# Optimization experiments

Measured on AMD Instinct MI355X. Metric: run time of the kernel, lower is better.

The kernel has to match this reference:

```python
import jax, jax.numpy as jnp
import numpy as np

BIG_NEG = -1.0e9
B, T, D, C, NF, K = 16, 2048, 64, 32, 16, 20


def setup_inputs() -> dict:
    key = jax.random.key(0)
    ks = jax.random.split(key, 8)
    return {
        "features": jax.random.normal(ks[0], (B, T, D), dtype=jnp.float32),
        "projection_matrix": jax.random.normal(ks[1], (D, NF), dtype=jnp.float32),
        "transition_embs_left": jax.random.normal(ks[2], (C, D), dtype=jnp.float32) * (1.0 / np.sqrt(D)),
        "transition_embs_right": jax.random.normal(ks[3], (C, D), dtype=jnp.float32) * (1.0 / np.sqrt(D)),
        "gaussian_means": jax.random.normal(ks[4], (C, D), dtype=jnp.float32) * 0.1,
        "gaussian_std": jnp.ones((D,), dtype=jnp.float32),
        "poisson_log_rates": jax.random.normal(ks[5], (C,), dtype=jnp.float32) * 0.1,
        "init_logits": jax.random.uniform(ks[6], (C,), dtype=jnp.float32),
        "max_k": K,
    }


def reference(features, projection_matrix, transition_embs_left,
              transition_embs_right, gaussian_means, gaussian_std,
              poisson_log_rates, init_logits, max_k):
    b, t, d = features.shape
    c = gaussian_means.shape[0]

    # --- diagonal-Gaussian per-frame emission log-probs: (B, T, C) ---
    inv_var = 1.0 / (gaussian_std * gaussian_std)              # (D,)
    xx = jnp.einsum("btd,d->bt", features * features, inv_var)  # (B,T)
    xm = jnp.einsum("btd,cd->btc", features, gaussian_means * inv_var)
    mm = jnp.einsum("cd,d->c", gaussian_means * gaussian_means, inv_var)
    quad = xx[:, :, None] - 2.0 * xm + mm[None, None, :]
    log_norm = -jnp.sum(jnp.log(gaussian_std)) - 0.5 * d * jnp.log(2.0 * jnp.pi)
    emission = -0.5 * quad + log_norm                           # (B,T,C)

    # --- sliding-window span sums over lengths 1..max_k (cumsum trick,
    # same math as the unfold+sum in sliding_sum) ---
    cs = jnp.concatenate(
        [jnp.zeros((b, 1, c), dtype=emission.dtype),
         jnp.cumsum(emission, axis=1)], axis=1)                 # (B,T+1,C)
    klens = jnp.arange(1, max_k + 1)                            # (K,)
    ends = jnp.arange(1, t + 1)                                 # (T,)
    starts = ends[None, :] - klens[:, None]                     # (K,T)
    valid = starts >= 0
    span = cs[:, None, ends, :] - jnp.take(cs, jnp.clip(starts, 0), axis=1)
    span = jnp.where(valid[None, :, :, None], span, BIG_NEG)    # (B,K,T,C)

    # --- Poisson length log-pmf per class: (K, C) ---
    kk = klens.astype(emission.dtype)
    length_lp = (kk[:, None] * poisson_log_rates[None, :]
                 - jnp.exp(poisson_log_rates)[None, :]
                 - jax.scipy.special.gammaln(kk + 1.0)[:, None])
    span_scores = span + length_lp[None, :, None, :]            # (B,K,T,C)

    # --- kernelized transition potentials (Performer-style projection;
    # the original kernel creator returns the plain bmm projection) ---
    left = transition_embs_left @ projection_matrix             # (C,NF)
    right = transition_embs_right @ projection_matrix           # (C,NF)
    trans_lp = jax.nn.log_softmax(right @ left.T, axis=0)       # (C_tgt, C_src)

    init_lp = jax.nn.log_softmax(init_logits)                   # (C,)
    return span_scores, trans_lp, init_lp
```

## Files before the change

### kernel.cpp

```cpp
#include <hip/hip_runtime.h>
#include <math.h>

#define BIG_NEG (-1.0e9f)

constexpr int B = 16, T = 2048, D = 64, C = 32, NF = 16;

typedef float f32x4 __attribute__((ext_vector_type(4)));

template<int KT, bool EXACT>
__global__ __launch_bounds__(256) void megakernel(
    const float* __restrict__ feat,
    const float* __restrict__ P,
    const float* __restrict__ TL,
    const float* __restrict__ TR,
    const float* __restrict__ STD,
    const float* __restrict__ MEANS,
    const float* __restrict__ PLR,
    const float* __restrict__ LOGITS,
    float* __restrict__ out,
    float* __restrict__ out_trans,
    float* __restrict__ out_init,
    int Krt)
{
    constexpr int RTOT = 64 + KT;
    constexpr int RPS  = (RTOT + 7) / 8;

    __shared__ float fs[RTOT * 64];
    __shared__ float wm_lds[C * 68];
    __shared__ float iv_lds[64];
    __shared__ float E[RTOT * 33];
    __shared__ float sllp[KT * C];
    __shared__ float slncc[C];
    __shared__ float red[8 * 33];
    __shared__ float lgam[32];
    __shared__ float scc[C];
    __shared__ float sln;

    const int bid = blockIdx.x;
    const int tid = threadIdx.x;
    const int KRUN = EXACT ? KT : Krt;

    if (bid < 512) {
        const int b  = bid & 15;
        const int t0 = (bid >> 4) << 6;

        const float* fb = feat + (size_t)b * T * D;
        constexpr int NF4 = RTOT * 16;
#pragma unroll
        for (int it = 0; it < (NF4 + 255) / 256; ++it) {
            const int idx4 = tid + it * 256;
            if (idx4 < NF4) {
                const int fi  = idx4 * 4;
                const int row = fi >> 6;
                const int col = fi & 63;
                const int t   = t0 - KT + row;
                f32x4 v = {0.f, 0.f, 0.f, 0.f};
                if (t >= 0) v = *(const f32x4*)(fb + (size_t)t * D + col);
                const int cswz = col ^ (((row >> 2) & 7) << 2);
                *(f32x4*)(fs + row * 64 + cswz) = v;
            }
        }
#pragma unroll
        for (int it = 0; it < 2; ++it) {
            const int idx = tid * 4 + it * 1024;
            const int c = idx >> 6, d = idx & 63;
            const f32x4 m = *(const f32x4*)(MEANS + idx);
            const f32x4 s = *(const f32x4*)(STD + d);
            f32x4 w = {m.x / (s.x * s.x), m.y / (s.y * s.y),
                       m.z / (s.z * s.z), m.w / (s.w * s.w)};
            *(f32x4*)(wm_lds + c * 68 + d) = w;
        }
        if (tid < 16) {
            const f32x4 s = *(const f32x4*)(STD + tid * 4);
            f32x4 v = {1.f / (s.x * s.x), 1.f / (s.y * s.y),
                       1.f / (s.z * s.z), 1.f / (s.w * s.w)};
            *(f32x4*)(iv_lds + tid * 4) = v;
        }
        if (tid < 32) {
            float x = (tid >= 1) ? logf((float)(tid + 1)) : 0.f;
#pragma unroll
            for (int off = 1; off < 32; off <<= 1) {
                float vv = __shfl_up(x, off, 64);
                if (tid >= off) x += vv;
            }
            lgam[tid] = x;
        } else if (tid >= 64 && tid < 128) {
            const int l = tid - 64;
            float lg = logf(STD[l]);
#pragma unroll
            for (int off = 1; off < 64; off <<= 1) lg += __shfl_xor(lg, off, 64);
            if (l == 0) sln = -lg - 58.81206612510332f;
        } else if (tid >= 192 && tid < 224) {
            const int c = tid - 192;
            float acc = 0.f;
#pragma unroll
            for (int dq = 0; dq < 64; dq += 4) {
                const f32x4 m = *(const f32x4*)(MEANS + c * 64 + dq);
                const f32x4 s = *(const f32x4*)(STD + dq);
                acc += (m.x * m.x) / (s.x * s.x) + (m.y * m.y) / (s.y * s.y)
                     + (m.z * m.z) / (s.z * s.z) + (m.w * m.w) / (s.w * s.w);
            }
            scc[c] = -0.5f * acc;
        }
        __syncthreads();

        const int j = tid >> 4;
        const float* wr0 = wm_lds + (2 * j) * 68;
        const float* wr1 = wr0 + 68;
#pragma unroll
        for (int pass = 0; pass < 2; ++pass) {
            const int i = (tid & 15) + pass * 16;
            if (pass == 0 || (tid & 15) < (KT / 4)) {
                const int swz = (i & 7) << 2;
                float a0[4] = {0,0,0,0}, a1[4] = {0,0,0,0}, xx[4] = {0,0,0,0};
#pragma unroll
                for (int q = 0; q < 16; ++q) {
                    const int dq = q * 4;
                    const f32x4 w0  = *(const f32x4*)(wr0 + dq);
                    const f32x4 w1  = *(const f32x4*)(wr1 + dq);
                    const f32x4 iv4 = *(const f32x4*)(iv_lds + dq);
                    const int cswz = dq ^ swz;
#pragma unroll
                    for (int tt = 0; tt < 4; ++tt) {
                        const f32x4 f = *(const f32x4*)(fs + (4*i+tt)*64 + cswz);
                        a0[tt] = fmaf(f.x, w0.x, a0[tt]); a0[tt] = fmaf(f.y, w0.y, a0[tt]);
                        a0[tt] = fmaf(f.z, w0.z, a0[tt]); a0[tt] = fmaf(f.w, w0.w, a0[tt]);
                        a1[tt] = fmaf(f.x, w1.x, a1[tt]); a1[tt] = fmaf(f.y, w1.y, a1[tt]);
                        a1[tt] = fmaf(f.z, w1.z, a1[tt]); a1[tt] = fmaf(f.w, w1.w, a1[tt]);
                        xx[tt] = fmaf(f.x * iv4.x, f.x, xx[tt]);
                        xx[tt] = fmaf(f.y * iv4.y, f.y, xx[tt]);
                        xx[tt] = fmaf(f.z * iv4.z, f.z, xx[tt]);
                        xx[tt] = fmaf(f.w * iv4.w, f.w, xx[tt]);
                    }
                }
#pragma unroll
                for (int tt = 0; tt < 4; ++tt) {
                    E[(4*i+tt) * 33 + 2*j]     = a0[tt] - 0.5f * xx[tt];
                    E[(4*i+tt) * 33 + 2*j + 1] = a1[tt] - 0.5f * xx[tt];
                }
            }
        }
        if (tid < C) slncc[tid] = sln + scc[tid];
        for (int e = tid; e < KRUN * C; e += 256) {
            const int k = e >> 5, c = e & 31;
            const float plr = PLR[c];
            sllp[e] = (float)(k + 1) * (plr + sln + scc[c]) - expf(plr) - lgam[k];
        }
        __syncthreads();

        {
            const int c = tid & 31, s = tid >> 5;
            float incl[RPS];
            float run = 0.f;
#pragma unroll
            for (int q = 0; q < RPS; ++q) {
                const int r = s * RPS + q;
                const float v = (r < RTOT) ? E[r * 33 + c] : 0.f;
                run += v;
                incl[q] = run;
            }
            red[s * 33 + c] = run;
            __syncthreads();
            float off = 0.f;
#pragma unroll
            for (int s2 = 0; s2 < 7; ++s2) off += (s2 < s) ? red[s2 * 33 + c] : 0.f;
            float* slds = fs;
            if (s == 0) slds[c] = 0.f;
#pragma unroll
            for (int q = 0; q < RPS; ++q) {
                const int r = s * RPS + q;
                if (r < RTOT) slds[(r + 1) * 32 + c] = off + incl[q];
            }
        }
        __syncthreads();

        const float* slds = fs;
        const int c4 = (tid & 7) << 2;
        const int tb = tid >> 3;
        const int ja = tb + KT;
        const int jb = ja + 32;
        const int ta = t0 + tb;
        const int tbg = t0 + 32 + tb;

        const f32x4 ea = *(const f32x4*)&slds[(ja + 1) * 32 + c4];
        const f32x4 eb = *(const f32x4*)&slds[(jb + 1) * 32 + c4];
        const f32x4 ln4 = *(const f32x4*)&slncc[c4];

        float* ob = out + ((size_t)(b * KRUN) * T + t0) * C + c4;
#pragma unroll
        for (int k = 0; k < KRUN; ++k) {
            const f32x4 lv = *(const f32x4*)&sllp[k * 32 + c4];
            const f32x4 sa = *(const f32x4*)&slds[(ja - k) * 32 + c4];
            const f32x4 sb = *(const f32x4*)&slds[(jb - k) * 32 + c4];
            const f32x4 mk = BIG_NEG - (float)(k + 1) * ln4;
            f32x4 ra = ea - sa + lv;
            f32x4 rb = eb - sb + lv;
            if (ta < k) ra = mk + lv;
            if (tbg < k) rb = mk + lv;
            float* op = ob + (size_t)k * T * C;
            *(f32x4*)(op + tb * C) = ra;
            *(f32x4*)(op + (32 + tb) * C) = rb;
        }

    } else if (bid == 512) {
        float* left  = fs;
        float* right = fs + 512;
        float* M     = fs + 1024;
        float* lse   = fs + 2112;
        for (int e = tid; e < C * NF; e += 256) {
            int cc = e >> 4, f = e & (NF - 1);
            float aL = 0.f, aR = 0.f;
            for (int d = 0; d < D; ++d) {
                float p = P[d * NF + f];
                aL = fmaf(TL[cc * D + d], p, aL);
                aR = fmaf(TR[cc * D + d], p, aR);
            }
            left[cc * NF + f] = aL;
            right[cc * NF + f] = aR;
        }
        __syncthreads();
        for (int e = tid; e < C * C; e += 256) {
            int i = e >> 5, jj = e & 31;
            float acc = 0.f;
            for (int f = 0; f < NF; ++f)
                acc = fmaf(right[i * NF + f], left[jj * NF + f], acc);
            M[i * 33 + jj] = acc;
        }
        __syncthreads();
        if (tid < C) {
            float mx = -INFINITY;
            for (int i = 0; i < C; ++i) mx = fmaxf(mx, M[i * 33 + tid]);
            float s = 0.f;
            for (int i = 0; i < C; ++i) s += expf(M[i * 33 + tid] - mx);
            lse[tid] = logf(s) + mx;
        }
        __syncthreads();
        for (int e = tid; e < C * C; e += 256)
            out_trans[e] = M[(e >> 5) * 33 + (e & 31)] - lse[e & 31];

    } else {
        if (tid < 32) {
            float vv = LOGITS[tid];
            float mx = vv;
#pragma unroll
            for (int off = 1; off < 32; off <<= 1)
                mx = fmaxf(mx, __shfl_xor(mx, off, 64));
            float s = expf(vv - mx);
#pragma unroll
            for (int off = 1; off < 32; off <<= 1) s += __shfl_xor(s, off, 64);
            out_init[tid] = vv - mx - logf(s);
        }
    }
}

extern "C" void kernel_launch(void* const* d_in, const int* in_sizes, int n_in,
                              void* d_out, int out_size, void* d_ws, size_t ws_size,
                              hipStream_t stream) {
    const float* feat   = (const float*)d_in[0];
    const float* P      = (const float*)d_in[1];
    const float* TL     = (const float*)d_in[2];
    const float* TR     = (const float*)d_in[3];
    const float* MEANS  = (const float*)d_in[4];
    const float* STDV   = (const float*)d_in[5];
    const float* PLR    = (const float*)d_in[6];
    const float* LOGITS = (const float*)d_in[7];

    const int K = (out_size - (C * C + C)) / (B * T * C);

    float* out       = (float*)d_out;
    float* out_trans = out + (size_t)B * K * T * C;
    float* out_init  = out_trans + C * C;

    if (K == 20) {
        megakernel<20, true><<<514, 256, 0, stream>>>(
            feat, P, TL, TR, STDV, MEANS, PLR, LOGITS,
            out, out_trans, out_init, K);
    } else if (K == 16) {
        megakernel<16, true><<<514, 256, 0, stream>>>(
            feat, P, TL, TR, STDV, MEANS, PLR, LOGITS,
            out, out_trans, out_init, K);
    } else if (K == 24) {
        megakernel<24, true><<<514, 256, 0, stream>>>(
            feat, P, TL, TR, STDV, MEANS, PLR, LOGITS,
            out, out_trans, out_init, K);
    } else {
        megakernel<32, false><<<514, 256, 0, stream>>>(
            feat, P, TL, TR, STDV, MEANS, PLR, LOGITS,
            out, out_trans, out_init, K);
    }
}
```

Baseline: 29.48 us.

## Halve time tile per block to 32 rows and split out squared-norm computation

```diff
diff --git a/kernel.cpp b/kernel.cpp
--- a/kernel.cpp
+++ b/kernel.cpp
@@ -22,13 +22,15 @@
     float* __restrict__ out_init,
     int Krt)
 {
-    constexpr int RTOT = 64 + KT;
+    constexpr int RTOT = 32 + KT;
+    constexpr int NQ   = (RTOT + 3) / 4;
     constexpr int RPS  = (RTOT + 7) / 8;
 
     __shared__ float fs[RTOT * 64];
     __shared__ float wm_lds[C * 68];
     __shared__ float iv_lds[64];
     __shared__ float E[RTOT * 33];
+    __shared__ float xxl[RTOT];
     __shared__ float sllp[KT * C];
     __shared__ float slncc[C];
     __shared__ float red[8 * 33];
@@ -40,9 +42,9 @@
     const int tid = threadIdx.x;
     const int KRUN = EXACT ? KT : Krt;
 
-    if (bid < 512) {
+    if (bid < 1024) {
         const int b  = bid & 15;
-        const int t0 = (bid >> 4) << 6;
+        const int t0 = (bid >> 4) << 5;
 
         const float* fb = feat + (size_t)b * T * D;
         constexpr int NF4 = RTOT * 16;
@@ -104,21 +106,18 @@
         }
         __syncthreads();
 
-        const int j = tid >> 4;
-        const float* wr0 = wm_lds + (2 * j) * 68;
-        const float* wr1 = wr0 + 68;
-#pragma unroll
-        for (int pass = 0; pass < 2; ++pass) {
-            const int i = (tid & 15) + pass * 16;
-            if (pass == 0 || (tid & 15) < (KT / 4)) {
+        {
+            const int i = tid & 15, j = tid >> 4;
+            if (i < NQ) {
                 const int swz = (i & 7) << 2;
-                float a0[4] = {0,0,0,0}, a1[4] = {0,0,0,0}, xx[4] = {0,0,0,0};
+                const float* wr0 = wm_lds + (2 * j) * 68;
+                const float* wr1 = wr0 + 68;
+                float a0[4] = {0,0,0,0}, a1[4] = {0,0,0,0};
 #pragma unroll
                 for (int q = 0; q < 16; ++q) {
                     const int dq = q * 4;
-                    const f32x4 w0  = *(const f32x4*)(wr0 + dq);
-                    const f32x4 w1  = *(const f32x4*)(wr1 + dq);
-                    const f32x4 iv4 = *(const f32x4*)(iv_lds + dq);
+                    const f32x4 w0 = *(const f32x4*)(wr0 + dq);
+                    const f32x4 w1 = *(const f32x4*)(wr1 + dq);
                     const int cswz = dq ^ swz;
 #pragma unroll
                     for (int tt = 0; tt < 4; ++tt) {
@@ -127,18 +126,30 @@
                         a0[tt] = fmaf(f.z, w0.z, a0[tt]); a0[tt] = fmaf(f.w, w0.w, a0[tt]);
                         a1[tt] = fmaf(f.x, w1.x, a1[tt]); a1[tt] = fmaf(f.y, w1.y, a1[tt]);
                         a1[tt] = fmaf(f.z, w1.z, a1[tt]); a1[tt] = fmaf(f.w, w1.w, a1[tt]);
-                        xx[tt] = fmaf(f.x * iv4.x, f.x, xx[tt]);
-                        xx[tt] = fmaf(f.y * iv4.y, f.y, xx[tt]);
-                        xx[tt] = fmaf(f.z * iv4.z, f.z, xx[tt]);
-                        xx[tt] = fmaf(f.w * iv4.w, f.w, xx[tt]);
                     }
                 }
 #pragma unroll
                 for (int tt = 0; tt < 4; ++tt) {
-                    E[(4*i+tt) * 33 + 2*j]     = a0[tt] - 0.5f * xx[tt];
-                    E[(4*i+tt) * 33 + 2*j + 1] = a1[tt] - 0.5f * xx[tt];
+                    E[(4*i+tt) * 33 + 2*j]     = a0[tt];
+                    E[(4*i+tt) * 33 + 2*j + 1] = a1[tt];
                 }
             }
+        }
+        if (tid < RTOT) {
+            const int row = tid;
+            const int swz = ((row >> 2) & 7) << 2;
+            float xx = 0.f;
+#pragma unroll
+            for (int q = 0; q < 16; ++q) {
+                const int dq = q * 4;
+                const f32x4 f   = *(const f32x4*)(fs + row * 64 + (dq ^ swz));
+                const f32x4 iv4 = *(const f32x4*)(iv_lds + dq);
+                xx = fmaf(f.x * iv4.x, f.x, xx);
+                xx = fmaf(f.y * iv4.y, f.y, xx);
+                xx = fmaf(f.z * iv4.z, f.z, xx);
+                xx = fmaf(f.w * iv4.w, f.w, xx);
+            }
+            xxl[row] = xx;
         }
         if (tid < C) slncc[tid] = sln + scc[tid];
         for (int e = tid; e < KRUN * C; e += 256) {
@@ -155,7 +166,7 @@
 #pragma unroll
             for (int q = 0; q < RPS; ++q) {
                 const int r = s * RPS + q;
-                const float v = (r < RTOT) ? E[r * 33 + c] : 0.f;
+                const float v = (r < RTOT) ? (E[r * 33 + c] - 0.5f * xxl[r]) : 0.f;
                 run += v;
                 incl[q] = run;
             }
@@ -164,45 +175,37 @@
             float off = 0.f;
 #pragma unroll
             for (int s2 = 0; s2 < 7; ++s2) off += (s2 < s) ? red[s2 * 33 + c] : 0.f;
-            float* slds = fs;
-            if (s == 0) slds[c] = 0.f;
+            float* S = fs;
+            if (s == 0) S[c] = 0.f;
 #pragma unroll
             for (int q = 0; q < RPS; ++q) {
                 const int r = s * RPS + q;
-                if (r < RTOT) slds[(r + 1) * 32 + c] = off + incl[q];
-            }
-        }
-        __syncthreads();
-
-        const float* slds = fs;
+                if (r < RTOT) S[(r + 1) * 32 + c] = off + incl[q];
+            }
+        }
+        __syncthreads();
+
+        const float* S = fs;
         const int c4 = (tid & 7) << 2;
         const int tb = tid >> 3;
         const int ja = tb + KT;
-        const int jb = ja + 32;
         const int ta = t0 + tb;
-        const int tbg = t0 + 32 + tb;
-
-        const f32x4 ea = *(const f32x4*)&slds[(ja + 1) * 32 + c4];
-        const f32x4 eb = *(const f32x4*)&slds[(jb + 1) * 32 + c4];
+
+        const f32x4 ea  = *(const f32x4*)&S[(ja + 1) * 32 + c4];
         const f32x4 ln4 = *(const f32x4*)&slncc[c4];
 
         float* ob = out + ((size_t)(b * KRUN) * T + t0) * C + c4;
 #pragma unroll
         for (int k = 0; k < KRUN; ++k) {
             const f32x4 lv = *(const f32x4*)&sllp[k * 32 + c4];
-            const f32x4 sa = *(const f32x4*)&slds[(ja - k) * 32 + c4];
-            const f32x4 sb = *(const f32x4*)&slds[(jb - k) * 32 + c4];
+            const f32x4 sa = *(const f32x4*)&S[(ja - k) * 32 + c4];
             const f32x4 mk = BIG_NEG - (float)(k + 1) * ln4;
             f32x4 ra = ea - sa + lv;
-            f32x4 rb = eb - sb + lv;
             if (ta < k) ra = mk + lv;
-            if (tbg < k) rb = mk + lv;
-            float* op = ob + (size_t)k * T * C;
-            *(f32x4*)(op + tb * C) = ra;
-            *(f32x4*)(op + (32 + tb) * C) = rb;
-        }
-
-    } else if (bid == 512) {
+            *(f32x4*)(ob + (size_t)k * T * C + tb * C) = ra;
+        }
+
+    } else if (bid == 1024) {
         float* left  = fs;
         float* right = fs + 512;
         float* M     = fs + 1024;
@@ -272,19 +275,19 @@
     float* out_init  = out_trans + C * C;
 
     if (K == 20) {
-        megakernel<20, true><<<514, 256, 0, stream>>>(
+        megakernel<20, true><<<1026, 256, 0, stream>>>(
             feat, P, TL, TR, STDV, MEANS, PLR, LOGITS,
             out, out_trans, out_init, K);
     } else if (K == 16) {
-        megakernel<16, true><<<514, 256, 0, stream>>>(
+        megakernel<16, true><<<1026, 256, 0, stream>>>(
             feat, P, TL, TR, STDV, MEANS, PLR, LOGITS,
             out, out_trans, out_init, K);
     } else if (K == 24) {
-        megakernel<24, true><<<514, 256, 0, stream>>>(
+        megakernel<24, true><<<1026, 256, 0, stream>>>(
             feat, P, TL, TR, STDV, MEANS, PLR, LOGITS,
             out, out_trans, out_init, K);
     } else {
-        megakernel<32, false><<<514, 256, 0, stream>>>(
+        megakernel<32, false><<<1026, 256, 0, stream>>>(
             feat, P, TL, TR, STDV, MEANS, PLR, LOGITS,
             out, out_trans, out_init, K);
     }
```

After: 31.11 us. 1.06x slower.

## Prefix-sum features first, then project cumsums with bf16 MFMA

Applied to the files above, without the earlier changes.

```diff
diff --git a/kernel.cpp b/kernel.cpp
--- a/kernel.cpp
+++ b/kernel.cpp
@@ -6,6 +6,14 @@
 constexpr int B = 16, T = 2048, D = 64, C = 32, NF = 16;
 
 typedef float f32x4 __attribute__((ext_vector_type(4)));
+using bf16x8 = __attribute__((ext_vector_type(8))) short;
+
+__device__ inline ushort f2bf(float x) {
+    union { float f; unsigned u; } cv; cv.f = x;
+    unsigned u = cv.u;
+    u += 0x7FFF + ((u >> 16) & 1);
+    return (ushort)(u >> 16);
+}
 
 template<int KT, bool EXACT>
 __global__ __launch_bounds__(256) void megakernel(
@@ -23,18 +31,41 @@
     int Krt)
 {
     constexpr int RTOT = 64 + KT;
-    constexpr int RPS  = (RTOT + 7) / 8;
-
-    __shared__ float fs[RTOT * 64];
-    __shared__ float wm_lds[C * 68];
-    __shared__ float iv_lds[64];
-    __shared__ float E[RTOT * 33];
-    __shared__ float sllp[KT * C];
-    __shared__ float slncc[C];
-    __shared__ float red[8 * 33];
-    __shared__ float lgam[32];
-    __shared__ float scc[C];
-    __shared__ float sln;
+    constexpr int ROWS = RTOT + 1;
+    constexpr int NT   = (ROWS + 15) / 16;
+    constexpr int CR   = RTOT / 4;
+    constexpr int XSEG = (RTOT + 7) / 8;
+
+    constexpr int OFF_FS   = 0;
+    constexpr int OFF_CSBF = OFF_FS + RTOT * 64;
+    constexpr int OFF_WMBF = OFF_CSBF + NT * 16 * 32;
+    constexpr int OFF_XX   = OFF_WMBF + 1152;
+    constexpr int OFF_CSXX = OFF_XX + RTOT;
+    constexpr int OFF_RED  = (OFF_CSXX + ROWS + 3) & ~3;
+    constexpr int OFF_RED2 = OFF_RED + 256;
+    constexpr int OFF_LLP  = OFF_RED2 + 8;
+    constexpr int OFF_LNCC = OFF_LLP + KT * 32;
+    constexpr int OFF_LGAM = OFF_LNCC + 32;
+    constexpr int OFF_SCC  = OFF_LGAM + 32;
+    constexpr int OFF_SLN  = OFF_SCC + 32;
+    constexpr int OFF_IV   = OFF_SLN + 4;
+    constexpr int SMEM_F32 = OFF_IV + 64;
+    __shared__ float smem[SMEM_F32];
+
+    float*  fs    = smem + OFF_FS;
+    float*  S     = smem + OFF_FS;
+    ushort* csbf  = (ushort*)(smem + OFF_CSBF);
+    ushort* wmb   = (ushort*)(smem + OFF_WMBF);
+    float*  xxl   = smem + OFF_XX;
+    float*  csxx  = smem + OFF_CSXX;
+    float*  red   = smem + OFF_RED;
+    float*  red2  = smem + OFF_RED2;
+    float*  sllp  = smem + OFF_LLP;
+    float*  slncc = smem + OFF_LNCC;
+    float*  lgam  = smem + OFF_LGAM;
+    float*  scc   = smem + OFF_SCC;
+    float*  slnp  = smem + OFF_SLN;
+    float*  ivp   = smem + OFF_IV;
 
     const int bid = blockIdx.x;
     const int tid = threadIdx.x;
@@ -62,19 +93,22 @@
         }
 #pragma unroll
         for (int it = 0; it < 2; ++it) {
-            const int idx = tid * 4 + it * 1024;
+            const int idx = (tid + it * 256) * 4;
             const int c = idx >> 6, d = idx & 63;
             const f32x4 m = *(const f32x4*)(MEANS + idx);
             const f32x4 s = *(const f32x4*)(STD + d);
-            f32x4 w = {m.x / (s.x * s.x), m.y / (s.y * s.y),
-                       m.z / (s.z * s.z), m.w / (s.w * s.w)};
-            *(f32x4*)(wm_lds + c * 68 + d) = w;
+            ushort4 u;
+            u.x = f2bf(m.x / (s.x * s.x));
+            u.y = f2bf(m.y / (s.y * s.y));
+            u.z = f2bf(m.z / (s.z * s.z));
+            u.w = f2bf(m.w / (s.w * s.w));
+            *(ushort4*)(wmb + c * 72 + d) = u;
         }
         if (tid < 16) {
             const f32x4 s = *(const f32x4*)(STD + tid * 4);
             f32x4 v = {1.f / (s.x * s.x), 1.f / (s.y * s.y),
                        1.f / (s.z * s.z), 1.f / (s.w * s.w)};
-            *(f32x4*)(iv_lds + tid * 4) = v;
+            *(f32x4*)(ivp + tid * 4) = v;
         }
         if (tid < 32) {
             float x = (tid >= 1) ? logf((float)(tid + 1)) : 0.f;
@@ -89,7 +123,7 @@
             float lg = logf(STD[l]);
 #pragma unroll
             for (int off = 1; off < 64; off <<= 1) lg += __shfl_xor(lg, off, 64);
-            if (l == 0) sln = -lg - 58.81206612510332f;
+            if (l == 0) *slnp = -lg - 58.81206612510332f;
         } else if (tid >= 192 && tid < 224) {
             const int c = tid - 192;
             float acc = 0.f;
@@ -104,77 +138,116 @@
         }
         __syncthreads();
 
-        const int j = tid >> 4;
-        const float* wr0 = wm_lds + (2 * j) * 68;
-        const float* wr1 = wr0 + 68;
-#pragma unroll
-        for (int pass = 0; pass < 2; ++pass) {
-            const int i = (tid & 15) + pass * 16;
-            if (pass == 0 || (tid & 15) < (KT / 4)) {
-                const int swz = (i & 7) << 2;
-                float a0[4] = {0,0,0,0}, a1[4] = {0,0,0,0}, xx[4] = {0,0,0,0};
-#pragma unroll
-                for (int q = 0; q < 16; ++q) {
-                    const int dq = q * 4;
-                    const f32x4 w0  = *(const f32x4*)(wr0 + dq);
-                    const f32x4 w1  = *(const f32x4*)(wr1 + dq);
-                    const f32x4 iv4 = *(const f32x4*)(iv_lds + dq);
-                    const int cswz = dq ^ swz;
-#pragma unroll
-                    for (int tt = 0; tt < 4; ++tt) {
-                        const f32x4 f = *(const f32x4*)(fs + (4*i+tt)*64 + cswz);
-                        a0[tt] = fmaf(f.x, w0.x, a0[tt]); a0[tt] = fmaf(f.y, w0.y, a0[tt]);
-                        a0[tt] = fmaf(f.z, w0.z, a0[tt]); a0[tt] = fmaf(f.w, w0.w, a0[tt]);
-                        a1[tt] = fmaf(f.x, w1.x, a1[tt]); a1[tt] = fmaf(f.y, w1.y, a1[tt]);
-                        a1[tt] = fmaf(f.z, w1.z, a1[tt]); a1[tt] = fmaf(f.w, w1.w, a1[tt]);
-                        xx[tt] = fmaf(f.x * iv4.x, f.x, xx[tt]);
-                        xx[tt] = fmaf(f.y * iv4.y, f.y, xx[tt]);
-                        xx[tt] = fmaf(f.z * iv4.z, f.z, xx[tt]);
-                        xx[tt] = fmaf(f.w * iv4.w, f.w, xx[tt]);
-                    }
+        const int col = tid & 63, seg = tid >> 6;
+        float loc[CR];
+        {
+            float runp = 0.f;
+#pragma unroll
+            for (int q = 0; q < CR; ++q) {
+                const int row = seg * CR + q;
+                const float v = fs[row * 64 + (col ^ (((row >> 2) & 7) << 2))];
+                loc[q] = v;
+                runp += v;
+            }
+            red[seg * 64 + col] = runp;
+        }
+        if (tid < RTOT) {
+            const int row = tid;
+            const int swz = ((row >> 2) & 7) << 2;
+            float xx = 0.f;
+#pragma unroll
+            for (int q = 0; q < 16; ++q) {
+                const int dq = q * 4;
+                const f32x4 f   = *(const f32x4*)(fs + row * 64 + (dq ^ swz));
+                const f32x4 iv4 = *(const f32x4*)(ivp + dq);
+                xx = fmaf(f.x * iv4.x, f.x, xx);
+                xx = fmaf(f.y * iv4.y, f.y, xx);
+                xx = fmaf(f.z * iv4.z, f.z, xx);
+                xx = fmaf(f.w * iv4.w, f.w, xx);
+            }
+            xxl[row] = xx;
+        }
+        {
+            const float ln = *slnp;
+            if (tid < C) slncc[tid] = ln + scc[tid];
+            for (int e = tid; e < KRUN * C; e += 256) {
+                const int k = e >> 5, c = e & 31;
+                const float plr = PLR[c];
+                sllp[e] = (float)(k + 1) * (plr + ln + scc[c]) - expf(plr) - lgam[k];
+            }
+        }
+        __syncthreads();
+
+        {
+            float off = 0.f;
+#pragma unroll
+            for (int s2 = 0; s2 < 3; ++s2) off += (s2 < seg) ? red[s2 * 64 + col] : 0.f;
+            float run = off;
+#pragma unroll
+            for (int q = 0; q < CR; ++q) {
+                const int row = seg * CR + q;
+                csbf[row * 64 + (((col >> 3) ^ (row & 7)) << 3) + (col & 7)] = f2bf(run);
+                run += loc[q];
+            }
+            if (seg == 3)
+                csbf[RTOT * 64 + (((col >> 3) ^ (RTOT & 7)) << 3) + (col & 7)] = f2bf(run);
+        }
+        if (tid < 8) {
+            float r2 = 0.f;
+            for (int q = 0; q < XSEG; ++q) {
+                const int i = tid * XSEG + q;
+                if (i < RTOT) { csxx[i] = r2; r2 += xxl[i]; }
+            }
+            red2[tid] = r2;
+        }
+        __syncthreads();
+
+        if (tid < ROWS) {
+            const int r = tid;
+            if (r == RTOT) {
+                float t = 0.f;
+#pragma unroll
+                for (int s2 = 0; s2 < 8; ++s2) t += red2[s2];
+                csxx[r] = t;
+            } else {
+                const int sg = r / XSEG;
+                float o = 0.f;
+#pragma unroll
+                for (int s2 = 0; s2 < 8; ++s2) o += (s2 < sg) ? red2[s2] : 0.f;
+                csxx[r] = csxx[r] + o;
+            }
+        }
+        {
+            const int l = tid & 63, wid = tid >> 6;
+            bf16x8 bfr[2][2];
+#pragma unroll
+            for (int ct = 0; ct < 2; ++ct)
+#pragma unroll
+                for (int h = 0; h < 2; ++h) {
+                    const int c  = ct * 16 + (l & 15);
+                    const int k0 = h * 32 + (l >> 4) * 8;
+                    bfr[ct][h] = *(const bf16x8*)(wmb + c * 72 + k0);
                 }
-#pragma unroll
-                for (int tt = 0; tt < 4; ++tt) {
-                    E[(4*i+tt) * 33 + 2*j]     = a0[tt] - 0.5f * xx[tt];
-                    E[(4*i+tt) * 33 + 2*j + 1] = a1[tt] - 0.5f * xx[tt];
+            for (int j = wid; j < NT * 2; j += 4) {
+                const int rt = j >> 1, ct = j & 1;
+                const int arow = rt * 16 + (l & 15);
+                const int kb = l >> 4;
+                const bf16x8 a0 = *(const bf16x8*)(csbf + arow * 64 + ((kb ^ (arow & 7)) << 3));
+                const bf16x8 a1 = *(const bf16x8*)(csbf + arow * 64 + (((4 + kb) ^ (arow & 7)) << 3));
+                f32x4 acc = {0.f, 0.f, 0.f, 0.f};
+                acc = __builtin_amdgcn_mfma_f32_16x16x32_bf16(a0, bfr[ct][0], acc, 0, 0, 0);
+                acc = __builtin_amdgcn_mfma_f32_16x16x32_bf16(a1, bfr[ct][1], acc, 0, 0, 0);
+                const int r0  = rt * 16 + (l >> 4) * 4;
+                const int cc0 = ct * 16 + (l & 15);
+#pragma unroll
+                for (int reg = 0; reg < 4; ++reg) {
+                    const int r = r0 + reg;
+                    if (r < ROWS) S[r * 36 + cc0] = acc[reg];
                 }
             }
         }
-        if (tid < C) slncc[tid] = sln + scc[tid];
-        for (int e = tid; e < KRUN * C; e += 256) {
-            const int k = e >> 5, c = e & 31;
-            const float plr = PLR[c];
-            sllp[e] = (float)(k + 1) * (plr + sln + scc[c]) - expf(plr) - lgam[k];
-        }
-        __syncthreads();
-
-        {
-            const int c = tid & 31, s = tid >> 5;
-            float incl[RPS];
-            float run = 0.f;
-#pragma unroll
-            for (int q = 0; q < RPS; ++q) {
-                const int r = s * RPS + q;
-                const float v = (r < RTOT) ? E[r * 33 + c] : 0.f;
-                run += v;
-                incl[q] = run;
-            }
-            red[s * 33 + c] = run;
-            __syncthreads();
-            float off = 0.f;
-#pragma unroll
-            for (int s2 = 0; s2 < 7; ++s2) off += (s2 < s) ? red[s2 * 33 + c] : 0.f;
-            float* slds = fs;
-            if (s == 0) slds[c] = 0.f;
-#pragma unroll
-            for (int q = 0; q < RPS; ++q) {
-                const int r = s * RPS + q;
-                if (r < RTOT) slds[(r + 1) * 32 + c] = off + incl[q];
-            }
-        }
-        __syncthreads();
-
-        const float* slds = fs;
+        __syncthreads();
+
         const int c4 = (tid & 7) << 2;
         const int tb = tid >> 3;
         const int ja = tb + KT;
@@ -182,19 +255,23 @@
         const int ta = t0 + tb;
         const int tbg = t0 + 32 + tb;
 
-        const f32x4 ea = *(const f32x4*)&slds[(ja + 1) * 32 + c4];
-        const f32x4 eb = *(const f32x4*)&slds[(jb + 1) * 32 + c4];
+        const f32x4 ea  = *(const f32x4*)&S[(ja + 1) * 36 + c4];
+        const f32x4 eb  = *(const f32x4*)&S[(jb + 1) * 36 + c4];
         const f32x4 ln4 = *(const f32x4*)&slncc[c4];
+        const float xea = csxx[ja + 1];
+        const float xeb = csxx[jb + 1];
 
         float* ob = out + ((size_t)(b * KRUN) * T + t0) * C + c4;
 #pragma unroll
         for (int k = 0; k < KRUN; ++k) {
             const f32x4 lv = *(const f32x4*)&sllp[k * 32 + c4];
-            const f32x4 sa = *(const f32x4*)&slds[(ja - k) * 32 + c4];
-            const f32x4 sb = *(const f32x4*)&slds[(jb - k) * 32 + c4];
+            const f32x4 sa = *(const f32x4*)&S[(ja - k) * 36 + c4];
+            const f32x4 sb = *(const f32x4*)&S[(jb - k) * 36 + c4];
+            const float dxa = xea - csxx[ja - k];
+            const float dxb = xeb - csxx[jb - k];
             const f32x4 mk = BIG_NEG - (float)(k + 1) * ln4;
-            f32x4 ra = ea - sa + lv;
-            f32x4 rb = eb - sb + lv;
+            f32x4 ra = ea - sa + (lv - 0.5f * dxa);
+            f32x4 rb = eb - sb + (lv - 0.5f * dxb);
             if (ta < k) ra = mk + lv;
             if (tbg < k) rb = mk + lv;
             float* op = ob + (size_t)k * T * C;
@@ -203,10 +280,10 @@
         }
 
     } else if (bid == 512) {
-        float* left  = fs;
-        float* right = fs + 512;
-        float* M     = fs + 1024;
-        float* lse   = fs + 2112;
+        float* left  = smem;
+        float* right = smem + 512;
+        float* M     = smem + 1024;
+        float* lse   = smem + 2112;
         for (int e = tid; e < C * NF; e += 256) {
             int cc = e >> 4, f = e & (NF - 1);
             float aL = 0.f, aR = 0.f;
```

Result: faster. 25.93 us (-12.1%).
